# Kernel tuning notes

Measured on AMD Instinct MI355X. Metric: run time of the kernel, lower is better.

The kernel has to match this reference:

```python
import jax, jax.numpy as jnp
import numpy as np


def setup_inputs() -> dict:
    key = jax.random.key(0)
    ks = jax.random.split(key, 6)
    B, S, E, H = 8, 2048, 1024, 64
    scale = 1.0 / np.sqrt(E)
    return {
        "query": jax.random.normal(ks[0], (B, S, E), dtype=jnp.float32),
        "key": jax.random.normal(ks[1], (B, S, E), dtype=jnp.float32),
        "value": jax.random.normal(ks[2], (B, S, E), dtype=jnp.float32),
        "Wq": jax.random.normal(ks[3], (E, H), dtype=jnp.float32) * scale,
        "bq": jnp.zeros((H,), dtype=jnp.float32),
        "Wk": jax.random.normal(ks[4], (E, H), dtype=jnp.float32) * scale,
        "bk": jnp.zeros((H,), dtype=jnp.float32),
        "Wv": jax.random.normal(ks[5], (E, H), dtype=jnp.float32) * scale,
        "bv": jnp.zeros((H,), dtype=jnp.float32),
    }


def reference(query, key, value, Wq, bq, Wk, bk, Wv, bv):
    # Linear projections: [B,S,E] @ [E,H] + [H] -> [B,S,H]
    q = jnp.einsum("bse,eh->bsh", query, Wq) + bq
    k = jnp.einsum("bse,eh->bsh", key, Wk) + bk
    v = jnp.einsum("bse,eh->bsh", value, Wv) + bv
    head_dim = q.shape[-1]
    # scores [B,S,S], softmax over last axis, then weighted sum of values
    scores = jnp.einsum("bqh,bkh->bqk", q, k) / jnp.sqrt(
        jnp.asarray(head_dim, dtype=q.dtype)
    )
    attn = jax.nn.softmax(scores, axis=-1)
    return jnp.einsum("bqk,bkh->bqh", attn, v)
```

## Files before the change

kernel.cpp:

```cpp
#include <hip/hip_runtime.h>
#include <math.h>

#define BB 8
#define SS 2048
#define EE 1024
#define HH 64
#define MM (BB * SS)

typedef unsigned short u16;
typedef __attribute__((ext_vector_type(8))) short short8;
typedef __attribute__((ext_vector_type(4))) float floatx4;

__device__ __forceinline__ u16 f2bf(float f) {
    union { float f; unsigned u; } a; a.f = f;
    unsigned r = a.u + 0x7fffu + ((a.u >> 16) & 1u);
    return (u16)(r >> 16);
}

__device__ __forceinline__ void split2(float f0, float f1, unsigned& hp, unsigned& lp) {
    union { float f; unsigned u; } a0, a1, h0, h1, l0, l1;
    a0.f = f0; a1.f = f1;
    h0.u = a0.u & 0xffff0000u;
    h1.u = a1.u & 0xffff0000u;
    l0.f = f0 - h0.f;
    l1.f = f1 - h1.f;
    hp = __builtin_amdgcn_perm(a1.u, a0.u, 0x07060302u);
    lp = __builtin_amdgcn_perm(l1.u, l0.u, 0x07060302u);
}

#define BM 128
#define BKp 64

__global__ __launch_bounds__(256) void proj_mfma(
    const float* __restrict__ A0, const float* __restrict__ A1, const float* __restrict__ A2,
    const float* __restrict__ W0, const float* __restrict__ W1, const float* __restrict__ W2,
    const float* __restrict__ b0, const float* __restrict__ b1, const float* __restrict__ b2,
    u16* __restrict__ o0, u16* __restrict__ o1, u16* __restrict__ o2)
{
    const int which = blockIdx.y;
    const float* __restrict__ A    = (which == 0) ? A0 : (which == 1) ? A1 : A2;
    const float* __restrict__ W    = (which == 0) ? W0 : (which == 1) ? W1 : W2;
    const float* __restrict__ bias = (which == 0) ? b0 : (which == 1) ? b1 : b2;
    u16* __restrict__ out          = (which == 0) ? o0 : (which == 1) ? o1 : o2;

    __shared__ __align__(16) u16 Ah[BM][72], Al[BM][72];
    __shared__ __align__(16) u16 Wh[64][72], Wl[64][72];

    const int tid  = threadIdx.x;
    const int lane = tid & 63;
    const int wave = tid >> 6;
    const int n    = lane & 15;
    const int g    = lane >> 4;
    const int row0 = blockIdx.x * BM;

    const int ar = tid >> 1;
    const int ak = (tid & 1) * 32;
    const int wk = (tid >> 4) * 4;
    const int wn = (tid & 15) * 4;

    floatx4 acc[2][4];
    #pragma unroll
    for (int mt = 0; mt < 2; ++mt)
        #pragma unroll
        for (int nt = 0; nt < 4; ++nt) acc[mt][nt] = (floatx4){0.f, 0.f, 0.f, 0.f};

    for (int kc = 0; kc < EE; kc += BKp) {
        const float* ap = A + (size_t)(row0 + ar) * EE + kc + ak;
        float4 av[8];
        #pragma unroll
        for (int i = 0; i < 8; ++i) av[i] = *(const float4*)(ap + i * 4);

        __syncthreads();

        #pragma unroll
        for (int i = 0; i < 4; ++i) {
            unsigned hp0, lp0, hp1, lp1, hp2, lp2, hp3, lp3;
            split2(av[2*i].x,   av[2*i].y,   hp0, lp0);
            split2(av[2*i].z,   av[2*i].w,   hp1, lp1);
            split2(av[2*i+1].x, av[2*i+1].y, hp2, lp2);
            split2(av[2*i+1].z, av[2*i+1].w, hp3, lp3);
            uint4 h4 = {hp0, hp1, hp2, hp3};
            uint4 l4 = {lp0, lp1, lp2, lp3};
            *(uint4*)&Ah[ar][ak + i * 8] = h4;
            *(uint4*)&Al[ar][ak + i * 8] = l4;
        }

        float4 wv[4];
        #pragma unroll
        for (int i = 0; i < 4; ++i)
            wv[i] = *(const float4*)&W[(size_t)(kc + wk + i) * HH + wn];
        #pragma unroll
        for (int j = 0; j < 4; ++j) {
            const float e0 = (&wv[0].x)[j], e1 = (&wv[1].x)[j],
                        e2 = (&wv[2].x)[j], e3 = (&wv[3].x)[j];
            unsigned hp0, lp0, hp1, lp1;
            split2(e0, e1, hp0, lp0);
            split2(e2, e3, hp1, lp1);
            uint2 h2 = {hp0, hp1};
            uint2 l2 = {lp0, lp1};
            *(uint2*)&Wh[wn + j][wk] = h2;
            *(uint2*)&Wl[wn + j][wk] = l2;
        }
        __syncthreads();

        #pragma unroll
        for (int ks = 0; ks < 2; ++ks) {
            short8 ahf[2], alf[2], whf[4], wlf[4];
            #pragma unroll
            for (int mt = 0; mt < 2; ++mt) {
                ahf[mt] = *(const short8*)&Ah[wave * 32 + mt * 16 + n][ks * 32 + g * 8];
                alf[mt] = *(const short8*)&Al[wave * 32 + mt * 16 + n][ks * 32 + g * 8];
            }
            #pragma unroll
            for (int nt = 0; nt < 4; ++nt) {
                whf[nt] = *(const short8*)&Wh[nt * 16 + n][ks * 32 + g * 8];
                wlf[nt] = *(const short8*)&Wl[nt * 16 + n][ks * 32 + g * 8];
            }
            #pragma unroll
            for (int mt = 0; mt < 2; ++mt)
                #pragma unroll
                for (int nt = 0; nt < 4; ++nt) {
                    acc[mt][nt] = __builtin_amdgcn_mfma_f32_16x16x32_bf16(ahf[mt], whf[nt], acc[mt][nt], 0, 0, 0);
                    acc[mt][nt] = __builtin_amdgcn_mfma_f32_16x16x32_bf16(alf[mt], whf[nt], acc[mt][nt], 0, 0, 0);
                    acc[mt][nt] = __builtin_amdgcn_mfma_f32_16x16x32_bf16(ahf[mt], wlf[nt], acc[mt][nt], 0, 0, 0);
                }
        }
    }

    #pragma unroll
    for (int mt = 0; mt < 2; ++mt)
        #pragma unroll
        for (int nt = 0; nt < 4; ++nt) {
            const float bv = bias[nt * 16 + n];
            #pragma unroll
            for (int r = 0; r < 4; ++r) {
                const int row = row0 + wave * 32 + mt * 16 + g * 4 + r;
                out[(size_t)row * HH + nt * 16 + n] = f2bf(acc[mt][nt][r] + bv);
            }
        }
}

__global__ __launch_bounds__(256) void flash_mfma(
    const u16* __restrict__ qp, const u16* __restrict__ kp,
    const u16* __restrict__ vp, float* __restrict__ out)
{
    __shared__ __align__(16) u16 Ks[2][64 * 64];
    __shared__ __align__(16) u16 Vt[2][64 * 64];
    __shared__ __align__(16) u16 Pw[4][16 * 72];

    const int b    = blockIdx.y;
    const int q0   = blockIdx.x * 32;
    const int tid  = threadIdx.x;
    const int lane = tid & 63;
    const int wave = tid >> 6;
    const int wq   = wave & 1;
    const int ks   = wave >> 1;
    const int n    = lane & 15;
    const int g    = lane >> 4;

    const u16* qrow = qp + ((size_t)b * SS + q0 + wq * 16 + n) * HH;
    const short8 qa0 = *(const short8*)(qrow + g * 8);
    const short8 qa1 = *(const short8*)(qrow + 32 + g * 8);

    floatx4 Oa[4];
    #pragma unroll
    for (int ht = 0; ht < 4; ++ht) Oa[ht] = (floatx4){0.f, 0.f, 0.f, 0.f};
    float m_i[4], l_i[4];
    #pragma unroll
    for (int r = 0; r < 4; ++r) { m_i[r] = -1e30f; l_i[r] = 0.f; }

    const u16* kb = kp + (size_t)b * SS * HH;
    const u16* vb = vp + (size_t)b * SS * HH;

    const int jK0 = tid >> 3, jK1 = 32 + (tid >> 3), cs = tid & 7;
    const int jV  = (tid & 15) * 4, hV = (tid >> 4) * 4;

    short8  kr0, kr1;
    ushort4 vr0, vr1, vr2, vr3;

    kr0 = *(const short8*)(kb + (size_t)jK0 * HH + cs * 8);
    kr1 = *(const short8*)(kb + (size_t)jK1 * HH + cs * 8);
    vr0 = *(const ushort4*)(vb + (size_t)(jV + 0) * HH + hV);
    vr1 = *(const ushort4*)(vb + (size_t)(jV + 1) * HH + hV);
    vr2 = *(const ushort4*)(vb + (size_t)(jV + 2) * HH + hV);
    vr3 = *(const ushort4*)(vb + (size_t)(jV + 3) * HH + hV);
    {
        *(short8*)&Ks[0][jK0 * 64 + ((cs ^ (jK0 & 7)) << 3)] = kr0;
        *(short8*)&Ks[0][jK1 * 64 + ((cs ^ (jK1 & 7)) << 3)] = kr1;
        const u16* a0 = (const u16*)&vr0; const u16* a1 = (const u16*)&vr1;
        const u16* a2 = (const u16*)&vr2; const u16* a3 = (const u16*)&vr3;
        #pragma unroll
        for (int i = 0; i < 4; ++i) {
            const int h = hV + i;
            ushort4 w; w.x = a0[i]; w.y = a1[i]; w.z = a2[i]; w.w = a3[i];
            *(ushort4*)((char*)&Vt[0][0] + h * 128 + (((jV >> 3) ^ (h & 7)) << 4) + ((jV & 4) << 1)) = w;
        }
    }
    __syncthreads();

    for (int t = 0; t < SS / 64; ++t) {
        const int cur = t & 1;

        if (t + 1 < SS / 64) {
            const size_t kt = (size_t)(t + 1) * 64;
            kr0 = *(const short8*)(kb + (kt + jK0) * HH + cs * 8);
            kr1 = *(const short8*)(kb + (kt + jK1) * HH + cs * 8);
            vr0 = *(const ushort4*)(vb + (kt + jV + 0) * HH + hV);
            vr1 = *(const ushort4*)(vb + (kt + jV + 1) * HH + hV);
            vr2 = *(const ushort4*)(vb + (kt + jV + 2) * HH + hV);
            vr3 = *(const ushort4*)(vb + (kt + jV + 3) * HH + hV);
        }

        floatx4 S[2];
        #pragma unroll
        for (int nt = 0; nt < 2; ++nt) {
            const int j = ks * 32 + nt * 16 + n;
            const short8 kf0 = *(const short8*)&Ks[cur][j * 64 + (((0 + g) ^ (j & 7)) << 3)];
            const short8 kf1 = *(const short8*)&Ks[cur][j * 64 + (((4 + g) ^ (j & 7)) << 3)];
            floatx4 a = (floatx4){0.f, 0.f, 0.f, 0.f};
            a = __builtin_amdgcn_mfma_f32_16x16x32_bf16(qa0, kf0, a, 0, 0, 0);
            a = __builtin_amdgcn_mfma_f32_16x16x32_bf16(qa1, kf1, a, 0, 0, 0);
            S[nt] = a;
        }

        float mx[4];
        #pragma unroll
        for (int r = 0; r < 4; ++r) mx[r] = -1e30f;
        #pragma unroll
        for (int nt = 0; nt < 2; ++nt)
            #pragma unroll
            for (int r = 0; r < 4; ++r) {
                S[nt][r] *= 0.125f;
                mx[r] = fmaxf(mx[r], S[nt][r]);
            }
        #pragma unroll
        for (int off = 8; off >= 1; off >>= 1)
            #pragma unroll
            for (int r = 0; r < 4; ++r)
                mx[r] = fmaxf(mx[r], __shfl_xor(mx[r], off, 64));

        float alpha[4], ps[4];
        #pragma unroll
        for (int r = 0; r < 4; ++r) {
            const float Mn = fmaxf(m_i[r], mx[r]);
            alpha[r] = __expf(m_i[r] - Mn);
            m_i[r]   = Mn;
            ps[r]    = 0.f;
        }
        float p[2][4];
        #pragma unroll
        for (int nt = 0; nt < 2; ++nt)
            #pragma unroll
            for (int r = 0; r < 4; ++r) {
                p[nt][r] = __expf(S[nt][r] - m_i[r]);
                ps[r] += p[nt][r];
            }
        #pragma unroll
        for (int off = 8; off >= 1; off >>= 1)
            #pragma unroll
            for (int r = 0; r < 4; ++r)
                ps[r] += __shfl_xor(ps[r], off, 64);
        #pragma unroll
        for (int r = 0; r < 4; ++r) l_i[r] = l_i[r] * alpha[r] + ps[r];
        #pragma unroll
        for (int ht = 0; ht < 4; ++ht)
            #pragma unroll
            for (int r = 0; r < 4; ++r) Oa[ht][r] *= alpha[r];

        #pragma unroll
        for (int nt = 0; nt < 2; ++nt)
            #pragma unroll
            for (int r = 0; r < 4; ++r)
                Pw[wave][(g * 4 + r) * 72 + nt * 16 + n] = f2bf(p[nt][r]);
        const short8 pa = *(const short8*)&Pw[wave][n * 72 + g * 8];

        #pragma unroll
        for (int ht = 0; ht < 4; ++ht) {
            const int h = ht * 16 + n;
            const short8 vf = *(const short8*)((const char*)&Vt[cur][0] + h * 128 +
                                               ((((ks << 2) + g) ^ (h & 7)) << 4));
            Oa[ht] = __builtin_amdgcn_mfma_f32_16x16x32_bf16(pa, vf, Oa[ht], 0, 0, 0);
        }

        if (t + 1 < SS / 64) {
            const int nx = cur ^ 1;
            *(short8*)&Ks[nx][jK0 * 64 + ((cs ^ (jK0 & 7)) << 3)] = kr0;
            *(short8*)&Ks[nx][jK1 * 64 + ((cs ^ (jK1 & 7)) << 3)] = kr1;
            const u16* a0 = (const u16*)&vr0; const u16* a1 = (const u16*)&vr1;
            const u16* a2 = (const u16*)&vr2; const u16* a3 = (const u16*)&vr3;
            #pragma unroll
            for (int i = 0; i < 4; ++i) {
                const int h = hV + i;
                ushort4 w; w.x = a0[i]; w.y = a1[i]; w.z = a2[i]; w.w = a3[i];
                *(ushort4*)((char*)&Vt[nx][0] + h * 128 + (((jV >> 3) ^ (h & 7)) << 4) + ((jV & 4) << 1)) = w;
            }
        }
        __syncthreads();
    }

    float* Cb = (float*)&Ks[0][0];
    float* Cm = Cb + 2 * 16 * 68;
    float* Cl = Cm + 32;
    if (ks == 1) {
        #pragma unroll
        for (int ht = 0; ht < 4; ++ht)
            #pragma unroll
            for (int r = 0; r < 4; ++r)
                Cb[(wq * 16 + g * 4 + r) * 68 + ht * 16 + n] = Oa[ht][r];
        if (n == 0)
            #pragma unroll
            for (int r = 0; r < 4; ++r) {
                Cm[wq * 16 + g * 4 + r] = m_i[r];
                Cl[wq * 16 + g * 4 + r] = l_i[r];
            }
    }
    __syncthreads();
    if (ks == 0) {
        float a0v[4], a1v[4], linv[4];
        #pragma unroll
        for (int r = 0; r < 4; ++r) {
            const int m = g * 4 + r;
            const float m1 = Cm[wq * 16 + m], l1 = Cl[wq * 16 + m];
            const float M  = fmaxf(m_i[r], m1);
            const float e0 = __expf(m_i[r] - M), e1 = __expf(m1 - M);
            a0v[r] = e0; a1v[r] = e1;
            linv[r] = 1.f / (l_i[r] * e0 + l1 * e1);
        }
        #pragma unroll
        for (int ht = 0; ht < 4; ++ht)
            #pragma unroll
            for (int r = 0; r < 4; ++r) {
                const float o1 = Cb[(wq * 16 + g * 4 + r) * 68 + ht * 16 + n];
                const float v  = (Oa[ht][r] * a0v[r] + o1 * a1v[r]) * linv[r];
                out[((size_t)b * SS + q0 + wq * 16 + g * 4 + r) * HH + ht * 16 + n] = v;
            }
    }
}

extern "C" void kernel_launch(void* const* d_in, const int* in_sizes, int n_in,
                              void* d_out, int out_size, void* d_ws, size_t ws_size,
                              hipStream_t stream) {
    const float* query = (const float*)d_in[0];
    const float* key   = (const float*)d_in[1];
    const float* value = (const float*)d_in[2];
    const float* Wq    = (const float*)d_in[3];
    const float* bq    = (const float*)d_in[4];
    const float* Wk    = (const float*)d_in[5];
    const float* bk    = (const float*)d_in[6];
    const float* Wv    = (const float*)d_in[7];
    const float* bv    = (const float*)d_in[8];
    float* out = (float*)d_out;

    u16* qp = (u16*)d_ws;
    u16* kp = qp + (size_t)MM * HH;
    u16* vp = kp + (size_t)MM * HH;

    dim3 pgrid(MM / BM, 3);
    proj_mfma<<<pgrid, 256, 0, stream>>>(query, key, value,
                                         Wq, Wk, Wv,
                                         bq, bk, bv,
                                         qp, kp, vp);

    dim3 agrid(SS / 32, BB);
    flash_mfma<<<agrid, 256, 0, stream>>>(qp, kp, vp, out);
}
```

Baseline: 287.7 us.

## Load A fragments straight to registers and double-buffer W in projection GEMM

```diff
diff --git a/kernel.cpp b/kernel.cpp
--- a/kernel.cpp
+++ b/kernel.cpp
@@ -28,8 +28,25 @@
     lp = __builtin_amdgcn_perm(l1.u, l0.u, 0x07060302u);
 }
 
-#define BM 128
-#define BKp 64
+#define BMROWS 64
+#define NCHUNK (EE / 64)
+
+__device__ __forceinline__ void stage_w(const float4* wv, int wk, int wn,
+                                        u16 (*__restrict__ wh)[72],
+                                        u16 (*__restrict__ wl)[72]) {
+    #pragma unroll
+    for (int j = 0; j < 4; ++j) {
+        const float e0 = (&wv[0].x)[j], e1 = (&wv[1].x)[j],
+                    e2 = (&wv[2].x)[j], e3 = (&wv[3].x)[j];
+        unsigned hp0, lp0, hp1, lp1;
+        split2(e0, e1, hp0, lp0);
+        split2(e2, e3, hp1, lp1);
+        uint2 h2 = {hp0, hp1};
+        uint2 l2 = {lp0, lp1};
+        *(uint2*)&wh[wn + j][wk] = h2;
+        *(uint2*)&wl[wn + j][wk] = l2;
+    }
+}
 
 __global__ __launch_bounds__(256) void proj_mfma(
     const float* __restrict__ A0, const float* __restrict__ A1, const float* __restrict__ A2,
@@ -43,101 +60,92 @@
     const float* __restrict__ bias = (which == 0) ? b0 : (which == 1) ? b1 : b2;
     u16* __restrict__ out          = (which == 0) ? o0 : (which == 1) ? o1 : o2;
 
-    __shared__ __align__(16) u16 Ah[BM][72], Al[BM][72];
-    __shared__ __align__(16) u16 Wh[64][72], Wl[64][72];
+    __shared__ __align__(16) u16 Wh[2][64][72], Wl[2][64][72];
 
     const int tid  = threadIdx.x;
     const int lane = tid & 63;
     const int wave = tid >> 6;
     const int n    = lane & 15;
     const int g    = lane >> 4;
-    const int row0 = blockIdx.x * BM;
-
-    const int ar = tid >> 1;
-    const int ak = (tid & 1) * 32;
+    const int row0 = blockIdx.x * BMROWS;
+
+    const float* __restrict__ ap = A + (size_t)(row0 + wave * 16 + n) * EE + g * 8;
+
     const int wk = (tid >> 4) * 4;
     const int wn = (tid & 15) * 4;
 
-    floatx4 acc[2][4];
-    #pragma unroll
-    for (int mt = 0; mt < 2; ++mt)
-        #pragma unroll
-        for (int nt = 0; nt < 4; ++nt) acc[mt][nt] = (floatx4){0.f, 0.f, 0.f, 0.f};
-
-    for (int kc = 0; kc < EE; kc += BKp) {
-        const float* ap = A + (size_t)(row0 + ar) * EE + kc + ak;
-        float4 av[8];
-        #pragma unroll
-        for (int i = 0; i < 8; ++i) av[i] = *(const float4*)(ap + i * 4);
-
+    floatx4 acc[4];
+    #pragma unroll
+    for (int nt = 0; nt < 4; ++nt) acc[nt] = (floatx4){0.f, 0.f, 0.f, 0.f};
+
+    float4 wv[4];
+    #pragma unroll
+    for (int i = 0; i < 4; ++i)
+        wv[i] = *(const float4*)&W[(size_t)(wk + i) * HH + wn];
+
+    float4 av[4];
+    av[0] = *(const float4*)(ap + 0);
+    av[1] = *(const float4*)(ap + 4);
+    av[2] = *(const float4*)(ap + 32);
+    av[3] = *(const float4*)(ap + 36);
+
+    stage_w(wv, wk, wn, Wh[0], Wl[0]);
+    __syncthreads();
+
+    for (int t = 0; t < NCHUNK; ++t) {
+        const int cur = t & 1;
+
+        float4 ac[4];
+        #pragma unroll
+        for (int i = 0; i < 4; ++i) ac[i] = av[i];
+
+        if (t + 1 < NCHUNK) {
+            const float* apn = ap + (t + 1) * 64;
+            av[0] = *(const float4*)(apn + 0);
+            av[1] = *(const float4*)(apn + 4);
+            av[2] = *(const float4*)(apn + 32);
+            av[3] = *(const float4*)(apn + 36);
+            #pragma unroll
+            for (int i = 0; i < 4; ++i)
+                wv[i] = *(const float4*)&W[(size_t)((t + 1) * 64 + wk + i) * HH + wn];
+        }
+
+        #pragma unroll
+        for (int ks = 0; ks < 2; ++ks) {
+            unsigned hp0, lp0, hp1, lp1, hp2, lp2, hp3, lp3;
+            split2(ac[ks * 2].x,     ac[ks * 2].y,     hp0, lp0);
+            split2(ac[ks * 2].z,     ac[ks * 2].w,     hp1, lp1);
+            split2(ac[ks * 2 + 1].x, ac[ks * 2 + 1].y, hp2, lp2);
+            split2(ac[ks * 2 + 1].z, ac[ks * 2 + 1].w, hp3, lp3);
+            union { uint4 u; short8 s; } ch, cl;
+            ch.u = (uint4){hp0, hp1, hp2, hp3};
+            cl.u = (uint4){lp0, lp1, lp2, lp3};
+            const short8 ah = ch.s, al = cl.s;
+
+            #pragma unroll
+            for (int nt = 0; nt < 4; ++nt) {
+                const short8 whf = *(const short8*)&Wh[cur][nt * 16 + n][ks * 32 + g * 8];
+                const short8 wlf = *(const short8*)&Wl[cur][nt * 16 + n][ks * 32 + g * 8];
+                acc[nt] = __builtin_amdgcn_mfma_f32_16x16x32_bf16(ah, whf, acc[nt], 0, 0, 0);
+                acc[nt] = __builtin_amdgcn_mfma_f32_16x16x32_bf16(al, whf, acc[nt], 0, 0, 0);
+                acc[nt] = __builtin_amdgcn_mfma_f32_16x16x32_bf16(ah, wlf, acc[nt], 0, 0, 0);
+            }
+        }
+
+        if (t + 1 < NCHUNK)
+            stage_w(wv, wk, wn, Wh[cur ^ 1], Wl[cur ^ 1]);
         __syncthreads();
-
-        #pragma unroll
-        for (int i = 0; i < 4; ++i) {
-            unsigned hp0, lp0, hp1, lp1, hp2, lp2, hp3, lp3;
-            split2(av[2*i].x,   av[2*i].y,   hp0, lp0);
-            split2(av[2*i].z,   av[2*i].w,   hp1, lp1);
-            split2(av[2*i+1].x, av[2*i+1].y, hp2, lp2);
-            split2(av[2*i+1].z, av[2*i+1].w, hp3, lp3);
-            uint4 h4 = {hp0, hp1, hp2, hp3};
-            uint4 l4 = {lp0, lp1, lp2, lp3};
-            *(uint4*)&Ah[ar][ak + i * 8] = h4;
-            *(uint4*)&Al[ar][ak + i * 8] = l4;
-        }
-
-        float4 wv[4];
-        #pragma unroll
-        for (int i = 0; i < 4; ++i)
-            wv[i] = *(const float4*)&W[(size_t)(kc + wk + i) * HH + wn];
-        #pragma unroll
-        for (int j = 0; j < 4; ++j) {
-            const float e0 = (&wv[0].x)[j], e1 = (&wv[1].x)[j],
-                        e2 = (&wv[2].x)[j], e3 = (&wv[3].x)[j];
-            unsigned hp0, lp0, hp1, lp1;
-            split2(e0, e1, hp0, lp0);
-            split2(e2, e3, hp1, lp1);
-            uint2 h2 = {hp0, hp1};
-            uint2 l2 = {lp0, lp1};
-            *(uint2*)&Wh[wn + j][wk] = h2;
-            *(uint2*)&Wl[wn + j][wk] = l2;
-        }
-        __syncthreads();
-
-        #pragma unroll
-        for (int ks = 0; ks < 2; ++ks) {
-            short8 ahf[2], alf[2], whf[4], wlf[4];
-            #pragma unroll
-            for (int mt = 0; mt < 2; ++mt) {
-                ahf[mt] = *(const short8*)&Ah[wave * 32 + mt * 16 + n][ks * 32 + g * 8];
-                alf[mt] = *(const short8*)&Al[wave * 32 + mt * 16 + n][ks * 32 + g * 8];
-            }
-            #pragma unroll
-            for (int nt = 0; nt < 4; ++nt) {
-                whf[nt] = *(const short8*)&Wh[nt * 16 + n][ks * 32 + g * 8];
-                wlf[nt] = *(const short8*)&Wl[nt * 16 + n][ks * 32 + g * 8];
-            }
-            #pragma unroll
-            for (int mt = 0; mt < 2; ++mt)
-                #pragma unroll
-                for (int nt = 0; nt < 4; ++nt) {
-                    acc[mt][nt] = __builtin_amdgcn_mfma_f32_16x16x32_bf16(ahf[mt], whf[nt], acc[mt][nt], 0, 0, 0);
-                    acc[mt][nt] = __builtin_amdgcn_mfma_f32_16x16x32_bf16(alf[mt], whf[nt], acc[mt][nt], 0, 0, 0);
-                    acc[mt][nt] = __builtin_amdgcn_mfma_f32_16x16x32_bf16(ahf[mt], wlf[nt], acc[mt][nt], 0, 0, 0);
-                }
-        }
-    }
-
-    #pragma unroll
-    for (int mt = 0; mt < 2; ++mt)
-        #pragma unroll
-        for (int nt = 0; nt < 4; ++nt) {
-            const float bv = bias[nt * 16 + n];
-            #pragma unroll
-            for (int r = 0; r < 4; ++r) {
-                const int row = row0 + wave * 32 + mt * 16 + g * 4 + r;
-                out[(size_t)row * HH + nt * 16 + n] = f2bf(acc[mt][nt][r] + bv);
-            }
-        }
+    }
+
+    #pragma unroll
+    for (int nt = 0; nt < 4; ++nt) {
+        const float bv = bias[nt * 16 + n];
+        #pragma unroll
+        for (int r = 0; r < 4; ++r) {
+            const int row = row0 + wave * 16 + g * 4 + r;
+            out[(size_t)row * HH + nt * 16 + n] = f2bf(acc[nt][r] + bv);
+        }
+    }
 }
 
 __global__ __launch_bounds__(256) void flash_mfma(
@@ -355,7 +363,7 @@
     u16* kp = qp + (size_t)MM * HH;
     u16* vp = kp + (size_t)MM * HH;
 
-    dim3 pgrid(MM / BM, 3);
+    dim3 pgrid(MM / BMROWS, 3);
     proj_mfma<<<pgrid, 256, 0, stream>>>(query, key, value,
                                          Wq, Wk, Wv,
                                          bq, bk, bv,
```

Measured after the change: 274.7 us. -4.5%, faster.
